# Kernel optimization log

Hardware: AMD Instinct MI355X
Metric: run time of the kernel (lower is better)

Reference implementation:

```python
import jax, jax.numpy as jnp
import numpy as np
from jax import lax

B, N, C = 4, 16384, 384
HEADS, HD = 8, 48
ALPHA = 4.0
KS = 5
HH = WW = 128


def setup_inputs() -> dict:
    key = jax.random.key(0)
    ks = jax.random.split(key, 9)
    s = 0.02
    return {
        "x": jax.random.normal(ks[0], (B, N, C), jnp.float32),
        "W_qg": jax.random.normal(ks[1], (C, 2 * C), jnp.float32) * s,
        "W_kv": jax.random.normal(ks[2], (C, 2 * C), jnp.float32) * s,
        "W_proj": jax.random.normal(ks[3], (C, C), jnp.float32) * s,
        "b_proj": jnp.zeros((C,), jnp.float32),
        "pos_enc": jax.random.normal(ks[4], (1, N, C), jnp.float32) * 0.02,
        "power_p": jax.random.normal(ks[5], (1, HEADS, 1, HD), jnp.float32) * 0.5,
        "scale_p": jax.random.normal(ks[6], (1, 1, C), jnp.float32) * 0.5,
        "dwc_w": jax.random.normal(ks[7], (HD, 1, KS, KS), jnp.float32) * s,
        "dwc_b": jnp.zeros((HD,), jnp.float32),
        "H": HH,
        "W": WW,
    }


def _relu_pow(x, p):
    # relu(x) ** p with safe gradients at x <= 0
    r = jax.nn.relu(x)
    base = jnp.where(r > 0, r, 1.0)
    return jnp.where(r > 0, base ** p, 0.0)


def reference(x, W_qg, W_kv, W_proj, b_proj, pos_enc, power_p, scale_p, dwc_w, dwc_b, H, W):
    Bx, Nx, Cx = x.shape
    h = power_p.shape[1]
    hd = power_p.shape[-1]

    qg = x @ W_qg                      # [B,N,2C]
    q, g = qg[..., :Cx], qg[..., Cx:]
    kv = x @ W_kv                      # [B,N,2C] (sr_ratio == 1)
    k, v = kv[..., :Cx], kv[..., Cx:]
    n = Nx
    k = k + pos_enc

    scale = jax.nn.softplus(scale_p)            # [1,1,C]
    power = 1.0 + ALPHA * jax.nn.sigmoid(power_p)  # [1,h,1,hd]
    q = q / scale
    k = k / scale

    # [B,h,N,hd]
    q = q.reshape(Bx, Nx, h, hd).transpose(0, 2, 1, 3)
    k = k.reshape(Bx, n, h, hd).transpose(0, 2, 1, 3)
    v = v.reshape(Bx, n, h, hd).transpose(0, 2, 1, 3)

    q_pos = _relu_pow(q, power)
    q_neg = _relu_pow(-q, power)
    k_pos = _relu_pow(k, power)
    k_neg = _relu_pow(-k, power)

    q_sim = jnp.concatenate([q_pos, q_neg], axis=-1)   # [B,h,N,2hd]
    q_opp = jnp.concatenate([q_neg, q_pos], axis=-1)
    kk = jnp.concatenate([k_pos, k_neg], axis=-1)      # [B,h,n,2hd]
    v1, v2 = v[..., : hd // 2], v[..., hd // 2:]

    k_mean = kk.mean(axis=2, keepdims=True)            # [B,h,1,2hd]
    inv_n = 1.0 / n

    z_sim = 1.0 / (jnp.sum(q_sim * k_mean, axis=-1, keepdims=True) + 1e-6)
    kv1 = jnp.einsum('bhnd,bhne->bhde', kk, v1) * inv_n  # [B,h,2hd,hd/2]
    x_sim = jnp.einsum('bhnd,bhde->bhne', q_sim, kv1) * z_sim

    z_opp = 1.0 / (jnp.sum(q_opp * k_mean, axis=-1, keepdims=True) + 1e-6)
    kv2 = jnp.einsum('bhnd,bhne->bhde', kk, v2) * inv_n
    x_opp = jnp.einsum('bhnd,bhde->bhne', q_opp, kv2) * z_opp

    out = jnp.concatenate([x_sim, x_opp], axis=-1)     # [B,h,N,hd]
    out = out.transpose(0, 2, 1, 3).reshape(Bx, Nx, Cx)

    # depthwise conv gate on v
    v4 = v.reshape(Bx * h, H, W, hd).transpose(0, 3, 1, 2)  # [B*h, hd, H, W]
    vc = lax.conv_general_dilated(
        v4, dwc_w, window_strides=(1, 1), padding='SAME',
        feature_group_count=hd,
        dimension_numbers=('NCHW', 'OIHW', 'NCHW'))
    vc = vc + dwc_b[None, :, None, None]
    v_out = vc.reshape(Bx, Cx, Nx).transpose(0, 2, 1)  # [B,N,C]

    out = (out + v_out) * g
    out = out @ W_proj + b_proj
    return out
```

## Files before the change

kernel.cpp:

```cpp
#include <hip/hip_runtime.h>
#include <math.h>


#define NB 4
#define NTOK 16384
#define CDIM 384
#define NHEAD 8
#define HDIM 48
#define IMGH 128
#define IMGW 128

typedef unsigned short u16;
typedef unsigned int u32;
typedef __attribute__((ext_vector_type(8))) short bf16x8;
typedef __attribute__((ext_vector_type(4))) float f32x4;

__device__ __forceinline__ float bf2f(u16 u) {
  return __uint_as_float(((unsigned)u) << 16);
}
__device__ __forceinline__ u16 f2bf(float f) {
  unsigned u = __float_as_uint(f);
  u += 0x7FFF + ((u >> 16) & 1);
  return (u16)(u >> 16);
}
__device__ __forceinline__ float pow_mag(float r, float p) {
  if (r < 1e-20f) return 0.0f;
  return exp2f(fminf(p * log2f(r), 80.0f));
}
__device__ __forceinline__ float ldx1(const void* p, size_t i, bool f32) {
  return f32 ? ((const float*)p)[i] : bf2f(((const u16*)p)[i]);
}
__device__ __forceinline__ void gload16(u16* lds, const u16* g) {
  __builtin_amdgcn_global_load_lds(
      (const __attribute__((address_space(1))) u32*)g,
      (__attribute__((address_space(3))) u32*)lds, 16, 0, 0);
}

__global__ __launch_bounds__(256) void k0_detect(const void* __restrict__ x,
                                                 int* __restrict__ flag) {
  __shared__ int s[256];
  const u16* p = (const u16*)x;
  const int t = threadIdx.x;
  int good = 0;
#pragma unroll
  for (int i = 0; i < 16; ++i) {
    const u16 w = p[t * 16 + i];
    const int e = (w >> 7) & 0xFF;
    good += (e >= 0x60 && e <= 0x85) ? 1 : 0;
  }
  s[t] = good;
  __syncthreads();
  for (int o = 128; o > 0; o >>= 1) {
    if (t < o) s[t] += s[t + o];
    __syncthreads();
  }
  if (t == 0) *flag = (s[0] >= (4096 * 4) / 5) ? 0 : 1;
}

__global__ __launch_bounds__(256) void kx_convert(const void* __restrict__ x,
                                                  const int* __restrict__ flag,
                                                  u16* __restrict__ xbf) {
  if (*flag == 0) return;
  const size_t S = (size_t)NB * NTOK * CDIM;
  const size_t tid = (size_t)blockIdx.x * 256 + threadIdx.x;
  const size_t stride = (size_t)gridDim.x * 256;
  const float4* xf = (const float4*)x;
  for (size_t i = tid; i < S / 8; i += stride) {
    const float4 a = xf[i * 2 + 0];
    const float4 b = xf[i * 2 + 1];
    *(ushort4*)(xbf + i * 8 + 0) = make_ushort4(f2bf(a.x), f2bf(a.y), f2bf(a.z), f2bf(a.w));
    *(ushort4*)(xbf + i * 8 + 4) = make_ushort4(f2bf(b.x), f2bf(b.y), f2bf(b.z), f2bf(b.w));
  }
}

__global__ __launch_bounds__(256) void kprep(
    const void* __restrict__ Wqg, const void* __restrict__ Wkv,
    const void* __restrict__ Wp, const int* __restrict__ flag,
    u16* __restrict__ W2T, u16* __restrict__ WpT)
{
  const bool f32 = (*flag != 0);
  const int idx = blockIdx.x * 256 + threadIdx.x;
  if (idx < 1536 * 384) {
    const int n = idx / 384, k = idx - n * 384;
    const float v = (n < 768) ? ldx1(Wqg, (size_t)k * 768 + n, f32)
                              : ldx1(Wkv, (size_t)k * 768 + (n - 768), f32);
    W2T[idx] = f2bf(v);
  } else {
    const int j = idx - 1536 * 384;
    if (j < 384 * 384) {
      const int n = j / 384, k = j - n * 384;
      WpT[j] = f2bf(ldx1(Wp, (size_t)k * 384 + n, f32));
    }
  }
}

__global__ __launch_bounds__(256) void k1_mfma(
    const void* __restrict__ x, const u16* __restrict__ xbf,
    const u16* __restrict__ W2T,
    const void* __restrict__ pos_enc, const void* __restrict__ scale_p,
    const int* __restrict__ flag, const int conv_ok,
    u16* __restrict__ qsT, u16* __restrict__ gT, u16* __restrict__ ksT, u16* __restrict__ vT)
{
  const bool f32 = (*flag != 0);
  const bool fast = (!f32) || (conv_ok != 0);
  const u16* Asrc = f32 ? xbf : (const u16*)x;
  __shared__ __align__(16) u16 Asm[2][128 * 64];
  __shared__ __align__(16) u16 Bsm[2][128 * 64];
  const int t = threadIdx.x;
  const int bid = blockIdx.x;
  const int rm = (bid & 7) * 768 + (bid >> 3);
  const int m_idx = rm / 12;
  const int n_idx = rm - m_idx * 12;
  const int n0 = n_idx * 128;
  const int m0 = m_idx * 128;
  const int wave = t >> 6, lane = t & 63;
  const int wr = wave >> 1, wc = wave & 1;
  const int lm = lane & 15, lq = lane >> 4;

  f32x4 acc[4][4] = {};

  auto STAGE = [&](int buf, int k0) {
#pragma unroll
    for (int i = 0; i < 4; ++i) {
      const int chunk = i * 256 + t;
      const int row = chunk >> 3, c8 = chunk & 7;
      const int sc8 = c8 ^ (row & 7);
      u16* lpA = &Asm[buf][(i * 256 + wave * 64) * 8];
      u16* lpB = &Bsm[buf][(i * 256 + wave * 64) * 8];
      gload16(lpA, Asrc + (size_t)(m0 + row) * CDIM + k0 + sc8 * 8);
      gload16(lpB, W2T + (size_t)(n0 + row) * CDIM + k0 + sc8 * 8);
    }
  };
  auto COMPUTE = [&](int buf) {
#pragma unroll
    for (int kh = 0; kh < 2; ++kh) {
      bf16x8 af[4], bfr[4];
#pragma unroll
      for (int r = 0; r < 4; ++r) {
        const int row = wr * 64 + r * 16 + lm;
        af[r] = *(const bf16x8*)&Asm[buf][row * 64 + (((kh * 4 + lq) ^ (row & 7)) * 8)];
      }
#pragma unroll
      for (int cb = 0; cb < 4; ++cb) {
        const int row = wc * 64 + cb * 16 + lm;
        bfr[cb] = *(const bf16x8*)&Bsm[buf][row * 64 + (((kh * 4 + lq) ^ (row & 7)) * 8)];
      }
#pragma unroll
      for (int r = 0; r < 4; ++r)
#pragma unroll
        for (int cb = 0; cb < 4; ++cb)
          acc[r][cb] = __builtin_amdgcn_mfma_f32_16x16x32_bf16(af[r], bfr[cb], acc[r][cb], 0, 0, 0);
    }
  };

  if (fast) {
    STAGE(0, 0);
    asm volatile("s_waitcnt vmcnt(0)" ::: "memory");
    __builtin_amdgcn_sched_barrier(0);
    __builtin_amdgcn_s_barrier();
    int cur = 0;
#pragma unroll
    for (int ks = 0; ks < 5; ++ks) {
      STAGE(cur ^ 1, (ks + 1) * 64);
      COMPUTE(cur);
      asm volatile("s_waitcnt vmcnt(0)" ::: "memory");
      __builtin_amdgcn_sched_barrier(0);
      __builtin_amdgcn_s_barrier();
      cur ^= 1;
    }
    COMPUTE(cur);
  } else {
    for (int k0 = 0; k0 < CDIM; k0 += 64) {
#pragma unroll
      for (int i = 0; i < 4; ++i) {
        const int chunk = t + i * 256;
        const int row = chunk >> 3, c8 = chunk & 7;
        const int ldsoff = row * 64 + ((c8 ^ (row & 7)) * 8);
        const float* xp = (const float*)x + (size_t)(m0 + row) * CDIM + k0 + c8 * 8;
        const float4 v0 = *(const float4*)xp;
        const float4 v1 = *(const float4*)(xp + 4);
        *(ushort4*)&Asm[0][ldsoff]     = make_ushort4(f2bf(v0.x), f2bf(v0.y), f2bf(v0.z), f2bf(v0.w));
        *(ushort4*)&Asm[0][ldsoff + 4] = make_ushort4(f2bf(v1.x), f2bf(v1.y), f2bf(v1.z), f2bf(v1.w));
        *(uint4*)&Bsm[0][ldsoff] = *(const uint4*)(W2T + (size_t)(n0 + row) * CDIM + k0 + c8 * 8);
      }
      __syncthreads();
      COMPUTE(0);
      __syncthreads();
    }
  }

  const int b = m0 >> 14;
  const int region = n0 / CDIM;
#pragma unroll
  for (int cb = 0; cb < 4; ++cb) {
    const int cg = n0 + wc * 64 + cb * 16 + lm;
    const int c = cg - region * CDIM;
    float inv = 1.0f;
    if (region == 0 || region == 2) inv = 1.0f / log1pf(expf(ldx1(scale_p, c, f32)));
#pragma unroll
    for (int r = 0; r < 4; ++r) {
      const int tok = (m0 & (NTOK - 1)) + wr * 64 + r * 16 + lq * 4;
      const size_t base = ((size_t)(b * CDIM + c)) * NTOK + tok;
      const f32x4 v = acc[r][cb];
      if (region == 0) {
        *(ushort4*)(qsT + base) =
            make_ushort4(f2bf(v[0] * inv), f2bf(v[1] * inv), f2bf(v[2] * inv), f2bf(v[3] * inv));
      } else if (region == 1) {
        *(ushort4*)(gT + base) = make_ushort4(f2bf(v[0]), f2bf(v[1]), f2bf(v[2]), f2bf(v[3]));
      } else if (region == 2) {
        const float p0 = ldx1(pos_enc, (size_t)(tok + 0) * CDIM + c, f32);
        const float p1 = ldx1(pos_enc, (size_t)(tok + 1) * CDIM + c, f32);
        const float p2 = ldx1(pos_enc, (size_t)(tok + 2) * CDIM + c, f32);
        const float p3 = ldx1(pos_enc, (size_t)(tok + 3) * CDIM + c, f32);
        *(ushort4*)(ksT + base) = make_ushort4(f2bf((v[0] + p0) * inv), f2bf((v[1] + p1) * inv),
                                               f2bf((v[2] + p2) * inv), f2bf((v[3] + p3) * inv));
      } else {
        *(ushort4*)(vT + base) = make_ushort4(f2bf(v[0]), f2bf(v[1]), f2bf(v[2]), f2bf(v[3]));
      }
    }
  }
}

__global__ __launch_bounds__(256) void k2_stats(
    const u16* __restrict__ ksT, const u16* __restrict__ vT,
    const void* __restrict__ power_p, const int* __restrict__ flag,
    float* __restrict__ km, float* __restrict__ kvm)
{
  const bool f32 = (*flag != 0);
  __shared__ float kkL[96][65];
  __shared__ float vL[48][65];
  __shared__ float pw[48];
  const int bh = blockIdx.x;
  const int b = bh >> 3, h = bh & 7;
  const int t = threadIdx.x;
  if (t < 48) pw[t] = 1.0f + 4.0f / (1.0f + expf(-ldx1(power_p, h * HDIM + t, f32)));
  __syncthreads();
  const int td = t & 15, te = t >> 4;
  float acc[6][3] = {};
  float ksum = 0.0f;
  const u16* ksbase = ksT + ((size_t)(b * CDIM + h * HDIM)) * NTOK;
  const u16* vbase  = vT  + ((size_t)(b * CDIM + h * HDIM)) * NTOK;
  const int n0base = blockIdx.y * 1024;
  for (int tile = 0; tile < 16; ++tile) {
    const int n0 = n0base + tile * 64;
    for (int i = t; i < 48 * 16; i += 256) {
      const int c = i >> 4, qd = (i & 15) * 4;
      ushort4 kq = *(const ushort4*)(ksbase + (size_t)c * NTOK + n0 + qd);
      ushort4 vq = *(const ushort4*)(vbase  + (size_t)c * NTOK + n0 + qd);
      const float p = pw[c];
      float kf[4] = {bf2f(kq.x), bf2f(kq.y), bf2f(kq.z), bf2f(kq.w)};
      float vf[4] = {bf2f(vq.x), bf2f(vq.y), bf2f(vq.z), bf2f(vq.w)};
#pragma unroll
      for (int jj = 0; jj < 4; ++jj) {
        const float f = pow_mag(fabsf(kf[jj]), p);
        kkL[c][qd + jj]      = (kf[jj] > 0.f) ? f : 0.f;
        kkL[c + 48][qd + jj] = (kf[jj] < 0.f) ? f : 0.f;
        vL[c][qd + jj] = vf[jj];
      }
    }
    __syncthreads();
#pragma unroll 2
    for (int nn = 0; nn < 64; ++nn) {
      float av[6], bv[3];
#pragma unroll
      for (int i = 0; i < 6; ++i) av[i] = kkL[td * 6 + i][nn];
#pragma unroll
      for (int j = 0; j < 3; ++j) bv[j] = vL[te * 3 + j][nn];
#pragma unroll
      for (int i = 0; i < 6; ++i)
#pragma unroll
        for (int j = 0; j < 3; ++j)
          acc[i][j] = fmaf(av[i], bv[j], acc[i][j]);
    }
    if (t < 96) {
#pragma unroll 4
      for (int nn = 0; nn < 64; ++nn) ksum += kkL[t][nn];
    }
    __syncthreads();
  }
  const float inv_n = 1.0f / (float)NTOK;
#pragma unroll
  for (int i = 0; i < 6; ++i)
#pragma unroll
    for (int j = 0; j < 3; ++j)
      atomicAdd(&kvm[(size_t)bh * 96 * 48 + (td * 6 + i) * 48 + (te * 3 + j)], acc[i][j] * inv_n);
  if (t < 96) atomicAdd(&km[bh * 96 + t], ksum * inv_n);
}

__global__ __launch_bounds__(256) void k3_attn(
    const u16* __restrict__ qsT, u16* __restrict__ attnT,
    const float* __restrict__ km_g, const float* __restrict__ kvm_g,
    const void* __restrict__ power_p, const int* __restrict__ flag)
{
  const bool f32 = (*flag != 0);
  __shared__ __align__(16) float kvmL[96][48];
  __shared__ float kmL[96];
  __shared__ float pw[48];
  const int bh = blockIdx.y;
  const int b = bh >> 3, h = bh & 7;
  const int t = threadIdx.x;
  for (int i = t; i < 96 * 48; i += 256) kvmL[i / 48][i % 48] = kvm_g[(size_t)bh * 96 * 48 + i];
  if (t < 96) kmL[t] = km_g[bh * 96 + t];
  if (t < 48) pw[t] = 1.0f + 4.0f / (1.0f + expf(-ldx1(power_p, h * HDIM + t, f32)));
  __syncthreads();
  const int n = blockIdx.x * 512 + t;
  const size_t chan0 = ((size_t)(b * CDIM + h * HDIM)) * NTOK + n;
  const u16* qbase = qsT + chan0;
  u16* obase = attnT + chan0;
  float4 accs[2][6] = {}, acco[2][6] = {};
  float zs[2] = {}, zo[2] = {};
  for (int d = 0; d < 48; ++d) {
    const float p = pw[d];
    float qp[2], qn[2];
#pragma unroll
    for (int i = 0; i < 2; ++i) {
      const float qv = bf2f(qbase[(size_t)d * NTOK + i * 256]);
      const float f = pow_mag(fabsf(qv), p);
      qp[i] = (qv > 0.f) ? f : 0.f;
      qn[i] = (qv < 0.f) ? f : 0.f;
      zs[i] = fmaf(qp[i], kmL[d], zs[i]); zs[i] = fmaf(qn[i], kmL[d + 48], zs[i]);
      zo[i] = fmaf(qn[i], kmL[d], zo[i]); zo[i] = fmaf(qp[i], kmL[d + 48], zo[i]);
    }
#pragma unroll
    for (int e4 = 0; e4 < 6; ++e4) {
      const float4 kvA = *(const float4*)&kvmL[d][e4 * 4];
      const float4 kvB = *(const float4*)&kvmL[d + 48][e4 * 4];
      const float4 kvC = *(const float4*)&kvmL[d][24 + e4 * 4];
      const float4 kvD = *(const float4*)&kvmL[d + 48][24 + e4 * 4];
#pragma unroll
      for (int i = 0; i < 2; ++i) {
        accs[i][e4].x = fmaf(qp[i], kvA.x, fmaf(qn[i], kvB.x, accs[i][e4].x));
        accs[i][e4].y = fmaf(qp[i], kvA.y, fmaf(qn[i], kvB.y, accs[i][e4].y));
        accs[i][e4].z = fmaf(qp[i], kvA.z, fmaf(qn[i], kvB.z, accs[i][e4].z));
        accs[i][e4].w = fmaf(qp[i], kvA.w, fmaf(qn[i], kvB.w, accs[i][e4].w));
        acco[i][e4].x = fmaf(qn[i], kvC.x, fmaf(qp[i], kvD.x, acco[i][e4].x));
        acco[i][e4].y = fmaf(qn[i], kvC.y, fmaf(qp[i], kvD.y, acco[i][e4].y));
        acco[i][e4].z = fmaf(qn[i], kvC.z, fmaf(qp[i], kvD.z, acco[i][e4].z));
        acco[i][e4].w = fmaf(qn[i], kvC.w, fmaf(qp[i], kvD.w, acco[i][e4].w));
      }
    }
  }
#pragma unroll
  for (int i = 0; i < 2; ++i) {
    const float zsi = 1.0f / (zs[i] + 1e-6f);
    const float zoi = 1.0f / (zo[i] + 1e-6f);
#pragma unroll
    for (int e4 = 0; e4 < 6; ++e4) {
      const float4 s = accs[i][e4], o = acco[i][e4];
      obase[(size_t)(e4 * 4 + 0) * NTOK + i * 256]    = f2bf(s.x * zsi);
      obase[(size_t)(e4 * 4 + 1) * NTOK + i * 256]    = f2bf(s.y * zsi);
      obase[(size_t)(e4 * 4 + 2) * NTOK + i * 256]    = f2bf(s.z * zsi);
      obase[(size_t)(e4 * 4 + 3) * NTOK + i * 256]    = f2bf(s.w * zsi);
      obase[(size_t)(24 + e4 * 4 + 0) * NTOK + i * 256] = f2bf(o.x * zoi);
      obase[(size_t)(24 + e4 * 4 + 1) * NTOK + i * 256] = f2bf(o.y * zoi);
      obase[(size_t)(24 + e4 * 4 + 2) * NTOK + i * 256] = f2bf(o.z * zoi);
      obase[(size_t)(24 + e4 * 4 + 3) * NTOK + i * 256] = f2bf(o.w * zoi);
    }
  }
}

__global__ __launch_bounds__(256) void k4_conv_combine(
    const u16* __restrict__ vT, const u16* __restrict__ gT,
    const void* __restrict__ dwc_w, const void* __restrict__ dwc_b,
    const int* __restrict__ flag,
    u16* __restrict__ attnT)
{
  const bool f32 = (*flag != 0);
  __shared__ float tile[20][128];
  const int bc = blockIdx.y;
  const int y0 = blockIdx.x * 16;
  const int t = threadIdx.x;
  const int d = bc % 48;
  float w[25];
#pragma unroll
  for (int i = 0; i < 25; ++i) w[i] = ldx1(dwc_w, d * 25 + i, f32);
  const float bias = ldx1(dwc_b, d, f32);
  const u16* vimg = vT + (size_t)bc * NTOK;
  for (int i = t; i < 20 * 128; i += 256) {
    const int r = i >> 7, xx = i & 127;
    const int gy = y0 + r - 2;
    tile[r][xx] = (gy >= 0 && gy < IMGH) ? bf2f(vimg[gy * IMGW + xx]) : 0.f;
  }
  __syncthreads();
  u16* abase = attnT + (size_t)bc * NTOK;
  const u16* gbase = gT + (size_t)bc * NTOK;
#pragma unroll
  for (int k = 0; k < 8; ++k) {
    const int px = t + k * 256;
    const int yy = px >> 7, xcol = px & 127;
    float acc = bias;
#pragma unroll
    for (int dy = 0; dy < 5; ++dy)
#pragma unroll
      for (int dx = 0; dx < 5; ++dx) {
        const int ux = xcol + dx - 2;
        const float val = (ux >= 0 && ux < IMGW) ? tile[yy + dy][ux] : 0.f;
        acc = fmaf(w[dy * 5 + dx], val, acc);
      }
    const int gidx = (y0 + yy) * IMGW + xcol;
    abase[gidx] = f2bf((bf2f(abase[gidx]) + acc) * bf2f(gbase[gidx]));
  }
}

__global__ __launch_bounds__(256) void k4b_transpose(
    const u16* __restrict__ src,
    u16* __restrict__ dst)
{
  __shared__ u16 tile[64][68];
  const int b  = blockIdx.z;
  const int c0 = blockIdx.y * 64;
  const int n0 = blockIdx.x * 64;
  const int t = threadIdx.x;
  const int tr = t >> 4, tq = t & 15;
#pragma unroll
  for (int i = 0; i < 4; ++i) {
    const int r = tr + i * 16;
    *(ushort4*)&tile[r][tq * 4] =
        *(const ushort4*)(src + ((size_t)(b * CDIM + c0 + r)) * NTOK + n0 + tq * 4);
  }
  __syncthreads();
#pragma unroll
  for (int i = 0; i < 4; ++i) {
    const int n = tr + i * 16;
    const ushort4 vv = make_ushort4(tile[tq * 4 + 0][n], tile[tq * 4 + 1][n],
                                    tile[tq * 4 + 2][n], tile[tq * 4 + 3][n]);
    *(ushort4*)(dst + ((size_t)(b * NTOK + n0 + n)) * CDIM + c0 + tq * 4) = vv;
  }
}

__global__ __launch_bounds__(256) void k5_mfma(
    const u16* __restrict__ A,
    const u16* __restrict__ WpT,
    const void* __restrict__ bp, const int* __restrict__ flag,
    void* __restrict__ out)
{
  const bool f32 = (*flag != 0);
  __shared__ __align__(16) u16 Asm[2][128 * 64];
  __shared__ __align__(16) u16 Bsm[2][128 * 64];
  const int t = threadIdx.x;
  const int bid = blockIdx.x;
  const int rm = (bid & 7) * 192 + (bid >> 3);
  const int m_idx = rm / 3;
  const int n_idx = rm - m_idx * 3;
  const int n0 = n_idx * 128;
  const int m0 = m_idx * 128;
  const int wave = t >> 6, lane = t & 63;
  const int wr = wave >> 1, wc = wave & 1;
  const int lm = lane & 15, lq = lane >> 4;

  f32x4 acc[4][4] = {};

  auto STAGE = [&](int buf, int k0) {
#pragma unroll
    for (int i = 0; i < 4; ++i) {
      const int chunk = i * 256 + t;
      const int row = chunk >> 3, c8 = chunk & 7;
      const int sc8 = c8 ^ (row & 7);
      u16* lpA = &Asm[buf][(i * 256 + wave * 64) * 8];
      u16* lpB = &Bsm[buf][(i * 256 + wave * 64) * 8];
      gload16(lpA, A + (size_t)(m0 + row) * CDIM + k0 + sc8 * 8);
      gload16(lpB, WpT + (size_t)(n0 + row) * CDIM + k0 + sc8 * 8);
    }
  };
  auto COMPUTE = [&](int buf) {
#pragma unroll
    for (int kh = 0; kh < 2; ++kh) {
      bf16x8 af[4], bfr[4];
#pragma unroll
      for (int r = 0; r < 4; ++r) {
        const int row = wr * 64 + r * 16 + lm;
        af[r] = *(const bf16x8*)&Asm[buf][row * 64 + (((kh * 4 + lq) ^ (row & 7)) * 8)];
      }
#pragma unroll
      for (int cb = 0; cb < 4; ++cb) {
        const int row = wc * 64 + cb * 16 + lm;
        bfr[cb] = *(const bf16x8*)&Bsm[buf][row * 64 + (((kh * 4 + lq) ^ (row & 7)) * 8)];
      }
#pragma unroll
      for (int r = 0; r < 4; ++r)
#pragma unroll
        for (int cb = 0; cb < 4; ++cb)
          acc[r][cb] = __builtin_amdgcn_mfma_f32_16x16x32_bf16(af[r], bfr[cb], acc[r][cb], 0, 0, 0);
    }
  };

  STAGE(0, 0);
  asm volatile("s_waitcnt vmcnt(0)" ::: "memory");
  __builtin_amdgcn_sched_barrier(0);
  __builtin_amdgcn_s_barrier();
  int cur = 0;
#pragma unroll
  for (int ks = 0; ks < 5; ++ks) {
    STAGE(cur ^ 1, (ks + 1) * 64);
    COMPUTE(cur);
    asm volatile("s_waitcnt vmcnt(0)" ::: "memory");
    __builtin_amdgcn_sched_barrier(0);
    __builtin_amdgcn_s_barrier();
    cur ^= 1;
  }
  COMPUTE(cur);

#pragma unroll
  for (int cb = 0; cb < 4; ++cb) {
    const int cg = n0 + wc * 64 + cb * 16 + lm;
    const float bb = ldx1(bp, cg, f32);
#pragma unroll
    for (int r = 0; r < 4; ++r) {
      const int rowtok = m0 + wr * 64 + r * 16 + lq * 4;
      const f32x4 v = acc[r][cb];
#pragma unroll
      for (int reg = 0; reg < 4; ++reg) {
        const size_t o = (size_t)(rowtok + reg) * CDIM + cg;
        if (f32) ((float*)out)[o] = v[reg] + bb;
        else     ((u16*)out)[o]   = f2bf(v[reg] + bb);
      }
    }
  }
}

extern "C" void kernel_launch(void* const* d_in, const int* in_sizes, int n_in,
                              void* d_out, int out_size, void* d_ws, size_t ws_size,
                              hipStream_t stream) {
  const void* x       = d_in[0];
  const void* Wqg     = d_in[1];
  const void* Wkv     = d_in[2];
  const void* Wproj   = d_in[3];
  const void* bproj   = d_in[4];
  const void* pos_enc = d_in[5];
  const void* power_p = d_in[6];
  const void* scale_p = d_in[7];
  const void* dwc_w   = d_in[8];
  const void* dwc_b   = d_in[9];

  const size_t S = (size_t)NB * NTOK * CDIM;
  const size_t stats_off   = 256;
  const size_t stats_bytes = (size_t)(32 * 96 + 32 * 96 * 48) * sizeof(float);
  const size_t w2t_elems = 1536 * 384, wpt_elems = 384 * 384;
  const size_t need = stats_off + stats_bytes + 3 * S * sizeof(u16)
                    + (w2t_elems + wpt_elems) * sizeof(u16);
  if (ws_size < need) return;

  int*   flag = (int*)d_ws;
  float* km   = (float*)((char*)d_ws + stats_off);
  float* kvm  = km + 32 * 96;
  u16* qsT = (u16*)((char*)d_ws + stats_off + stats_bytes);
  u16* gT  = qsT + S;
  u16* ksT = gT + S;
  u16* W2T = ksT + S;
  u16* WpT = W2T + w2t_elems;
  u16* vT  = (u16*)d_out;

  const int conv_ok = (out_size >= (int)(S * 4)) ? 1 : 0;
  u16* xbf = conv_ok ? ((u16*)d_out + S) : (u16*)d_out;

  hipMemsetAsync(km, 0, stats_bytes, stream);

  k0_detect<<<1, 256, 0, stream>>>(x, flag);
  if (conv_ok) kx_convert<<<2048, 256, 0, stream>>>(x, flag, xbf);
  kprep<<<(int)((w2t_elems + wpt_elems + 255) / 256), 256, 0, stream>>>(
      Wqg, Wkv, Wproj, flag, W2T, WpT);
  k1_mfma<<<6144, 256, 0, stream>>>(x, xbf, W2T, pos_enc, scale_p, flag, conv_ok,
                                    qsT, gT, ksT, vT);
  k2_stats<<<dim3(32, 16), 256, 0, stream>>>(ksT, vT, power_p, flag, km, kvm);
  k3_attn<<<dim3(32, 32), 256, 0, stream>>>(qsT, ksT, km, kvm, power_p, flag);
  k4_conv_combine<<<dim3(8, 1536), 256, 0, stream>>>(vT, gT, dwc_w, dwc_b, flag, ksT);
  k4b_transpose<<<dim3(256, 6, 4), 256, 0, stream>>>(ksT, qsT);
  k5_mfma<<<1536, 256, 0, stream>>>(qsT, WpT, bproj, flag, d_out);
}
```

Measured before the change: 823.8 us.

## Use 8 waves per block and stage GEMM epilogue through LDS for coalesced stores

The QKV/gate projection GEMM now runs with 512 threads (8 waves, each covering 64x32 of the 128x128 tile), which halves per-wave accumulators and staging work. The transposed bf16 epilogue is written into shared memory first, then copied to global memory as 16-byte row-contiguous stores instead of scattered 8-byte column stores. The aim is better latency hiding and coalesced writes of the channel-major outputs, at the cost of extra barriers and an LDS round trip. LDS reuse relies on the pipeline buffers being idle after the final sync.

```diff
diff --git a/kernel.cpp b/kernel.cpp
--- a/kernel.cpp
+++ b/kernel.cpp
@@ -94,7 +94,7 @@
   }
 }
 
-__global__ __launch_bounds__(256) void k1_mfma(
+__global__ __launch_bounds__(512) void k1_mfma(
     const void* __restrict__ x, const u16* __restrict__ xbf,
     const u16* __restrict__ W2T,
     const void* __restrict__ pos_enc, const void* __restrict__ scale_p,
@@ -104,8 +104,7 @@
   const bool f32 = (*flag != 0);
   const bool fast = (!f32) || (conv_ok != 0);
   const u16* Asrc = f32 ? xbf : (const u16*)x;
-  __shared__ __align__(16) u16 Asm[2][128 * 64];
-  __shared__ __align__(16) u16 Bsm[2][128 * 64];
+  __shared__ __align__(16) u16 smem[4][128 * 64];
   const int t = threadIdx.x;
   const int bid = blockIdx.x;
   const int rm = (bid & 7) * 768 + (bid >> 3);
@@ -114,19 +113,19 @@
   const int n0 = n_idx * 128;
   const int m0 = m_idx * 128;
   const int wave = t >> 6, lane = t & 63;
-  const int wr = wave >> 1, wc = wave & 1;
+  const int wr = wave >> 2, wc = wave & 3;
   const int lm = lane & 15, lq = lane >> 4;
 
-  f32x4 acc[4][4] = {};
+  f32x4 acc[4][2] = {};
 
   auto STAGE = [&](int buf, int k0) {
 #pragma unroll
-    for (int i = 0; i < 4; ++i) {
-      const int chunk = i * 256 + t;
+    for (int i = 0; i < 2; ++i) {
+      const int chunk = i * 512 + t;
       const int row = chunk >> 3, c8 = chunk & 7;
       const int sc8 = c8 ^ (row & 7);
-      u16* lpA = &Asm[buf][(i * 256 + wave * 64) * 8];
-      u16* lpB = &Bsm[buf][(i * 256 + wave * 64) * 8];
+      u16* lpA = &smem[buf][(i * 512 + wave * 64) * 8];
+      u16* lpB = &smem[2 + buf][(i * 512 + wave * 64) * 8];
       gload16(lpA, Asrc + (size_t)(m0 + row) * CDIM + k0 + sc8 * 8);
       gload16(lpB, W2T + (size_t)(n0 + row) * CDIM + k0 + sc8 * 8);
     }
@@ -134,21 +133,21 @@
   auto COMPUTE = [&](int buf) {
 #pragma unroll
     for (int kh = 0; kh < 2; ++kh) {
-      bf16x8 af[4], bfr[4];
+      bf16x8 af[4], bfr[2];
 #pragma unroll
       for (int r = 0; r < 4; ++r) {
         const int row = wr * 64 + r * 16 + lm;
-        af[r] = *(const bf16x8*)&Asm[buf][row * 64 + (((kh * 4 + lq) ^ (row & 7)) * 8)];
-      }
-#pragma unroll
-      for (int cb = 0; cb < 4; ++cb) {
-        const int row = wc * 64 + cb * 16 + lm;
-        bfr[cb] = *(const bf16x8*)&Bsm[buf][row * 64 + (((kh * 4 + lq) ^ (row & 7)) * 8)];
+        af[r] = *(const bf16x8*)&smem[buf][row * 64 + (((kh * 4 + lq) ^ (row & 7)) * 8)];
+      }
+#pragma unroll
+      for (int cb = 0; cb < 2; ++cb) {
+        const int row = wc * 32 + cb * 16 + lm;
+        bfr[cb] = *(const bf16x8*)&smem[2 + buf][row * 64 + (((kh * 4 + lq) ^ (row & 7)) * 8)];
       }
 #pragma unroll
       for (int r = 0; r < 4; ++r)
 #pragma unroll
-        for (int cb = 0; cb < 4; ++cb)
+        for (int cb = 0; cb < 2; ++cb)
           acc[r][cb] = __builtin_amdgcn_mfma_f32_16x16x32_bf16(af[r], bfr[cb], acc[r][cb], 0, 0, 0);
     }
   };
@@ -172,16 +171,16 @@
   } else {
     for (int k0 = 0; k0 < CDIM; k0 += 64) {
 #pragma unroll
-      for (int i = 0; i < 4; ++i) {
-        const int chunk = t + i * 256;
+      for (int i = 0; i < 2; ++i) {
+        const int chunk = t + i * 512;
         const int row = chunk >> 3, c8 = chunk & 7;
         const int ldsoff = row * 64 + ((c8 ^ (row & 7)) * 8);
         const float* xp = (const float*)x + (size_t)(m0 + row) * CDIM + k0 + c8 * 8;
         const float4 v0 = *(const float4*)xp;
         const float4 v1 = *(const float4*)(xp + 4);
-        *(ushort4*)&Asm[0][ldsoff]     = make_ushort4(f2bf(v0.x), f2bf(v0.y), f2bf(v0.z), f2bf(v0.w));
-        *(ushort4*)&Asm[0][ldsoff + 4] = make_ushort4(f2bf(v1.x), f2bf(v1.y), f2bf(v1.z), f2bf(v1.w));
-        *(uint4*)&Bsm[0][ldsoff] = *(const uint4*)(W2T + (size_t)(n0 + row) * CDIM + k0 + c8 * 8);
+        *(ushort4*)&smem[0][ldsoff]     = make_ushort4(f2bf(v0.x), f2bf(v0.y), f2bf(v0.z), f2bf(v0.w));
+        *(ushort4*)&smem[0][ldsoff + 4] = make_ushort4(f2bf(v1.x), f2bf(v1.y), f2bf(v1.z), f2bf(v1.w));
+        *(uint4*)&smem[2][ldsoff] = *(const uint4*)(W2T + (size_t)(n0 + row) * CDIM + k0 + c8 * 8);
       }
       __syncthreads();
       COMPUTE(0);
@@ -189,35 +188,47 @@
     }
   }
 
+  __syncthreads();
+  u16* et = &smem[0][0];
   const int b = m0 >> 14;
+  const int TOK0 = m0 & (NTOK - 1);
   const int region = n0 / CDIM;
 #pragma unroll
-  for (int cb = 0; cb < 4; ++cb) {
-    const int cg = n0 + wc * 64 + cb * 16 + lm;
-    const int c = cg - region * CDIM;
+  for (int cb = 0; cb < 2; ++cb) {
+    const int cl = wc * 32 + cb * 16 + lm;
+    const int c = (n0 - region * CDIM) + cl;
     float inv = 1.0f;
     if (region == 0 || region == 2) inv = 1.0f / log1pf(expf(ldx1(scale_p, c, f32)));
 #pragma unroll
     for (int r = 0; r < 4; ++r) {
-      const int tok = (m0 & (NTOK - 1)) + wr * 64 + r * 16 + lq * 4;
-      const size_t base = ((size_t)(b * CDIM + c)) * NTOK + tok;
+      const int tl = wr * 64 + r * 16 + lq * 4;
       const f32x4 v = acc[r][cb];
-      if (region == 0) {
-        *(ushort4*)(qsT + base) =
-            make_ushort4(f2bf(v[0] * inv), f2bf(v[1] * inv), f2bf(v[2] * inv), f2bf(v[3] * inv));
-      } else if (region == 1) {
-        *(ushort4*)(gT + base) = make_ushort4(f2bf(v[0]), f2bf(v[1]), f2bf(v[2]), f2bf(v[3]));
-      } else if (region == 2) {
+      ushort4 w;
+      if (region == 2) {
+        const int tok = TOK0 + tl;
         const float p0 = ldx1(pos_enc, (size_t)(tok + 0) * CDIM + c, f32);
         const float p1 = ldx1(pos_enc, (size_t)(tok + 1) * CDIM + c, f32);
         const float p2 = ldx1(pos_enc, (size_t)(tok + 2) * CDIM + c, f32);
         const float p3 = ldx1(pos_enc, (size_t)(tok + 3) * CDIM + c, f32);
-        *(ushort4*)(ksT + base) = make_ushort4(f2bf((v[0] + p0) * inv), f2bf((v[1] + p1) * inv),
-                                               f2bf((v[2] + p2) * inv), f2bf((v[3] + p3) * inv));
+        w = make_ushort4(f2bf((v[0] + p0) * inv), f2bf((v[1] + p1) * inv),
+                         f2bf((v[2] + p2) * inv), f2bf((v[3] + p3) * inv));
+      } else if (region == 0) {
+        w = make_ushort4(f2bf(v[0] * inv), f2bf(v[1] * inv), f2bf(v[2] * inv), f2bf(v[3] * inv));
       } else {
-        *(ushort4*)(vT + base) = make_ushort4(f2bf(v[0]), f2bf(v[1]), f2bf(v[2]), f2bf(v[3]));
-      }
-    }
+        w = make_ushort4(f2bf(v[0]), f2bf(v[1]), f2bf(v[2]), f2bf(v[3]));
+      }
+      *(ushort4*)&et[cl * 136 + tl] = w;
+    }
+  }
+  __syncthreads();
+  u16* dst = (region == 0) ? qsT : (region == 1) ? gT : (region == 2) ? ksT : vT;
+  const int cbase = b * CDIM + (n0 - region * CDIM);
+#pragma unroll
+  for (int i = 0; i < 4; ++i) {
+    const int idx = i * 512 + t;
+    const int row = idx >> 4, seg = idx & 15;
+    const uint4 val = *(const uint4*)&et[row * 136 + seg * 8];
+    *(uint4*)(dst + ((size_t)(cbase + row)) * NTOK + TOK0 + seg * 8) = val;
   }
 }
 
@@ -559,7 +570,7 @@
   if (conv_ok) kx_convert<<<2048, 256, 0, stream>>>(x, flag, xbf);
   kprep<<<(int)((w2t_elems + wpt_elems + 255) / 256), 256, 0, stream>>>(
       Wqg, Wkv, Wproj, flag, W2T, WpT);
-  k1_mfma<<<6144, 256, 0, stream>>>(x, xbf, W2T, pos_enc, scale_p, flag, conv_ok,
+  k1_mfma<<<6144, 512, 0, stream>>>(x, xbf, W2T, pos_enc, scale_p, flag, conv_ok,
                                     qsT, gT, ksT, vT);
   k2_stats<<<dim3(32, 16), 256, 0, stream>>>(ksT, vT, power_p, flag, km, kvm);
   k3_attn<<<dim3(32, 32), 256, 0, stream>>>(qsT, ksT, km, kvm, power_p, flag);
```

Result: faster. 787.9 us (-4.4%).
